# Kernel tuning notes

Measured on AMD Instinct MI355X. Metric: run time of the kernel, lower is better.

Reference implementation:

```python
import jax, jax.numpy as jnp
import numpy as np
from jax import lax

HEADS = 8
WIN = 4
SR = 4

def setup_inputs() -> dict:
    key = jax.random.key(0)
    ks = jax.random.split(key, 12)
    B, C, H, W = 8, 256, 64, 64
    def n(k, shape, s=0.02):
        return jax.random.normal(k, shape, jnp.float32) * s
    return {
        'x_bchw': jax.random.normal(ks[0], (B, C, H, W), jnp.float32),
        'W_lepe': n(ks[1], (C, C)), 'b_lepe': jnp.zeros((C,), jnp.float32),
        'conv_w': n(ks[2], (C, 1, 3, 3), 0.1), 'conv_b': jnp.zeros((C,), jnp.float32),
        'sr_w': n(ks[3], (C, C, SR, SR), 0.05), 'sr_b': jnp.zeros((C,), jnp.float32),
        'norm_g': jnp.ones((C,), jnp.float32), 'norm_b': jnp.zeros((C,), jnp.float32),
        'Wq1': n(ks[4], (C, C // 2)), 'Wkv1': n(ks[5], (C, C)),
        'Wq2': n(ks[6], (C, C // 2)), 'Wkv2': n(ks[7], (C, C)),
        'Wproj': n(ks[8], (C, C)), 'bproj': jnp.zeros((C,), jnp.float32),
        'sigma': jnp.array([2e-4], jnp.float32), 'magnitude': jnp.array([1e-2], jnp.float32),
    }

def _forward(x, W_lepe, b_lepe, conv_w, conv_b, sr_w, sr_b, norm_g, norm_b,
             Wq1, Wkv1, Wq2, Wkv2, Wproj, bproj, sigma, magnitude):
    B, C, H, W = x.shape
    N = H * W
    h2 = HEADS // 2
    d = C // HEADS
    scale = d ** -0.5
    dn = ('NCHW', 'OIHW', 'NCHW')

    tokens = x.reshape(B, C, N).transpose(0, 2, 1)  # [B,N,C]

    # LEPE: linear -> depthwise 3x3 conv
    lepe = tokens @ W_lepe + b_lepe
    lepe = lepe.transpose(0, 2, 1).reshape(B, C, H, W)
    lepe = lax.conv_general_dilated(lepe, conv_w, (1, 1), 'SAME',
                                    dimension_numbers=dn, feature_group_count=C)
    lepe = lepe + conv_b[None, :, None, None]
    lepe = lepe.reshape(B, C, N).transpose(0, 2, 1)  # [B,N,C]

    # --- global branch: spatially reduced KV ---
    q_g = (tokens @ Wq1).reshape(B, N, h2, d).transpose(0, 2, 1, 3)  # [B,h2,N,d]
    fr = lax.conv_general_dilated(x, sr_w, (SR, SR), 'VALID', dimension_numbers=dn)
    fr = fr + sr_b[None, :, None, None]
    Nr = (H // SR) * (W // SR)
    fr = fr.reshape(B, C, Nr).transpose(0, 2, 1)  # [B,Nr,C]
    mu = fr.mean(-1, keepdims=True)
    var = jnp.mean((fr - mu) ** 2, -1, keepdims=True)
    fr = (fr - mu) / jnp.sqrt(var + 1e-5) * norm_g + norm_b
    fr = jax.nn.gelu(fr, approximate=False)
    kv = (fr @ Wkv1).reshape(B, Nr, 2, h2, d)
    kg = kv[:, :, 0].transpose(0, 2, 1, 3)  # [B,h2,Nr,d]
    vg = kv[:, :, 1].transpose(0, 2, 1, 3)
    ag = jax.nn.softmax(jnp.einsum('bhnd,bhmd->bhnm', q_g, kg) * scale, axis=-1)
    xg = jnp.einsum('bhnm,bhmd->bhnd', ag, vg).transpose(0, 2, 1, 3).reshape(B, N, C // 2)
    gsig = lax.stop_gradient(ag).mean(1).mean(2).reshape(B, H, W)

    # --- local branch: 4x4 window attention ---
    qn = (tokens @ Wq2).reshape(B, N, h2, d).transpose(0, 2, 1, 3)
    kv2 = (tokens @ Wkv2).reshape(B, N, 2, h2, d)
    kl = kv2[:, :, 0].transpose(0, 2, 1, 3)
    vl = kv2[:, :, 1].transpose(0, 2, 1, 3)

    def wpart(t):
        return t.reshape(B * h2, H // WIN, WIN, W // WIN, WIN, d) \
                .transpose(0, 1, 3, 2, 4, 5).reshape(-1, WIN * WIN, d)

    al = jax.nn.softmax(jnp.einsum('wid,wjd->wij', wpart(qn), wpart(kl)) * scale, axis=-1)
    xl = jnp.einsum('wij,wjd->wid', al, wpart(vl))
    nW = (H // WIN) * (W // WIN)
    # window_reverse
    xl = xl.reshape(B, h2, H // WIN, W // WIN, WIN, WIN, d) \
           .transpose(0, 2, 4, 3, 5, 1, 6).reshape(B, N, h2 * d)
    lsig = lax.stop_gradient(al).reshape(B, h2, nW, WIN * WIN, WIN * WIN).mean(1).mean(2)
    lsig = lsig.reshape(B, H // WIN, W // WIN, WIN, WIN) \
               .transpose(0, 1, 3, 2, 4).reshape(B, H, W)

    fused = (jnp.concatenate([xg, xl], axis=-1) + lepe) @ Wproj + bproj  # [B,N,C]

    se = (lsig + gsig) * 0.5
    if H // SR == 16:  # static python condition -> apply Gaussian frequency bias (side=64)
        coord = jnp.arange(64, dtype=jnp.float32) - 31.5
        Xg, Yg = jnp.meshgrid(coord, coord, indexing='ij')
        Z = magnitude[0] * sigma[0] / (2.0 * np.pi) * jnp.exp(-0.5 * sigma[0] * (Xg * Xg + Yg * Yg)) + 1.0
        se = se * Z[None]
    se1 = se.reshape(B, N)
    se2 = se.transpose(0, 2, 1).reshape(B, N)
    return fused, se1, se2

def reference(x_bchw, W_lepe, b_lepe, conv_w, conv_b, sr_w, sr_b, norm_g, norm_b,
              Wq1, Wkv1, Wq2, Wkv2, Wproj, bproj, sigma, magnitude):
    return _forward(x_bchw, W_lepe, b_lepe, conv_w, conv_b, sr_w, sr_b, norm_g, norm_b,
                    Wq1, Wkv1, Wq2, Wkv2, Wproj, bproj, sigma, magnitude)
```

## Files before the change

kernel.cpp:

```cpp
#include <hip/hip_runtime.h>
#include <hip/hip_bf16.h>
#include <math.h>


#define SCALE 0.17677669529663687f
#define WFENCE() asm volatile("s_waitcnt lgkmcnt(0)" ::: "memory")

typedef unsigned short ush;
typedef __attribute__((ext_vector_type(8))) short s8v;
typedef __attribute__((ext_vector_type(4))) float f4v;

__device__ __forceinline__ float bf2f(ush u) {
    return __uint_as_float(((unsigned)u) << 16);
}
__device__ __forceinline__ ush f2bf(float f) {
    unsigned u = __float_as_uint(f);
    u += 0x7FFFu + ((u >> 16) & 1u);
    return (ush)(u >> 16);
}

__device__ __forceinline__ float ldfr(const void* b, size_t i, bool isbf) {
    return isbf ? bf2f(((const ush*)b)[i]) : ((const float*)b)[i];
}
__device__ __forceinline__ void ld8r(const void* b, size_t i, float* o, bool isbf) {
    if (isbf) {
        uint4 u = *reinterpret_cast<const uint4*>((const ush*)b + i);
        o[0] = bf2f((ush)u.x); o[1] = bf2f((ush)(u.x >> 16));
        o[2] = bf2f((ush)u.y); o[3] = bf2f((ush)(u.y >> 16));
        o[4] = bf2f((ush)u.z); o[5] = bf2f((ush)(u.z >> 16));
        o[6] = bf2f((ush)u.w); o[7] = bf2f((ush)(u.w >> 16));
    } else {
        const float4* p = reinterpret_cast<const float4*>((const float*)b + i);
        float4 a = p[0], c = p[1];
        o[0] = a.x; o[1] = a.y; o[2] = a.z; o[3] = a.w;
        o[4] = c.x; o[5] = c.y; o[6] = c.z; o[7] = c.w;
    }
}

struct US8 { ush s[8]; };
__device__ __forceinline__ US8 load8i(const ush* p) {
    uint4 u = *reinterpret_cast<const uint4*>(p);
    US8 r;
    r.s[0] = (ush)u.x; r.s[1] = (ush)(u.x >> 16);
    r.s[2] = (ush)u.y; r.s[3] = (ush)(u.y >> 16);
    r.s[4] = (ush)u.z; r.s[5] = (ush)(u.z >> 16);
    r.s[6] = (ush)u.w; r.s[7] = (ush)(u.w >> 16);
    return r;
}

__global__ __launch_bounds__(256) void prep(
        const void* x, const void* Wlepe, const void* Wq1, const void* Wq2,
        const void* Wkv2, const void* Wproj, const void* Wkv1, const void* blepe,
        const void* bproj, const void* convw, const void* convb, const void* srw,
        const void* srb, const void* ng, const void* nb,
        ush* tok, ush* wallt, ush* wprojt, ush* wkv1c, ush* wsrt, ush* bias_all,
        ush* bprojc, ush* convwc, ush* convbc, float* srbc, float* ngc, float* nbc) {
    bool isbf = (*(const unsigned*)ng) == 0x3F803F80u;
    __shared__ float T[32][33];
    int blk = blockIdx.x, t = threadIdx.x;
    if (blk < 768) {
        int n = blk;
        const void* s; int ncols, col;
        if (n < 256)      { s = Wlepe; ncols = 256; col = n; }
        else if (n < 384) { s = Wq1;   ncols = 128; col = n - 256; }
        else if (n < 512) { s = Wq2;   ncols = 128; col = n - 384; }
        else              { s = Wkv2;  ncols = 256; col = n - 512; }
        wallt[n * 256 + t] = f2bf(ldfr(s, (size_t)t * ncols + col, isbf));
    } else if (blk < 1024) {
        int n = blk - 768;
        wprojt[n * 256 + t] = f2bf(ldfr(Wproj, (size_t)t * 256 + n, isbf));
    } else if (blk == 1024) {
        bias_all[t]       = f2bf(ldfr(blepe, t, isbf));
        bias_all[256 + t] = 0;
        bias_all[512 + t] = 0;
        bprojc[t] = f2bf(ldfr(bproj, t, isbf));
        convbc[t] = f2bf(ldfr(convb, t, isbf));
        srbc[t] = ldfr(srb, t, isbf);
        ngc[t]  = ldfr(ng, t, isbf);
        nbc[t]  = ldfr(nb, t, isbf);
#pragma unroll
        for (int j = 0; j < 9; j++) convwc[j * 256 + t] = f2bf(ldfr(convw, t * 9 + j, isbf));
    } else if (blk < 1089) {
        int base = (blk - 1025) * 1024;
#pragma unroll
        for (int j = 0; j < 4; j++) {
            int e = base + j * 256 + t;
            wkv1c[e] = f2bf(ldfr(Wkv1, e, isbf));
        }
    } else if (blk < 1345) {
        int n = blk - 1089;
        float v[16];
        ld8r(srw, (size_t)n * 4096 + t * 16, v, isbf);
        ld8r(srw, (size_t)n * 4096 + t * 16 + 8, v + 8, isbf);
#pragma unroll
        for (int kyx = 0; kyx < 16; kyx++)
            wsrt[(size_t)n * 4096 + kyx * 256 + t] = f2bf(v[kyx]);
    } else {
        int blk2 = blk - 1345;
        int n0 = (blk2 & 127) * 32, c0 = ((blk2 >> 7) & 7) * 32, b = blk2 >> 10;
        int cl = t >> 5, nl = t & 31;
#pragma unroll
        for (int i = 0; i < 4; i++) {
            int c = c0 + cl + i * 8;
            T[cl + i * 8][nl] = ldfr(x, (((size_t)(b * 256 + c)) << 12) + n0 + nl, isbf);
        }
        __syncthreads();
        int cl2 = t & 31, nr = t >> 5;
#pragma unroll
        for (int i = 0; i < 4; i++) {
            int n = n0 + nr + i * 8;
            tok[(size_t)(b * 4096 + n) * 256 + c0 + cl2] = f2bf(T[cl2][nr + i * 8]);
        }
    }
}

__global__ __launch_bounds__(256) void big_gemm(const ush* __restrict__ tok,
                                                const ush* __restrict__ wsrt,
                                                const ush* __restrict__ wallt,
                                                const ush* __restrict__ bias_all,
                                                float* __restrict__ fr_part,
                                                ush* __restrict__ lepe_lin,
                                                ush* __restrict__ qg,
                                                ush* __restrict__ qn,
                                                ush* __restrict__ kv2) {
    __shared__ ush As[128][40];
    __shared__ ush Bs[128][40];
    int t = threadIdx.x, blk = blockIdx.x;
    int r = t >> 1, half = t & 1;
    int lane = t & 63, wv = t >> 6;
    int moff = (wv & 1) * 64, noff = (wv >> 1) * 64;
    int fm = lane & 15, q8 = (lane >> 4) * 8;
    int row4 = (lane >> 4) * 4;
    f4v acc[4][4] = {};
    if (blk < 128) {
        int m0 = (blk & 15) * 128, jt = (blk >> 4) & 1, kz = blk >> 5;
        int m = m0 + r;
        int b = m >> 8, p = m & 255;
        size_t abase = ((size_t)(b * 4096 + (p >> 4) * 256 + (p & 15) * 4)) * 256 + half * 16;
        const ush* bsrc = wsrt + (size_t)(jt * 128 + r) * 4096 + half * 16;
        for (int j = 0; j < 32; j++) {
            int k0 = kz * 1024 + j * 32;
            int kyx = k0 >> 8, ci0 = k0 & 255;
            int ky = kyx >> 2, kx = kyx & 3;
            const ush* asrc = tok + abase + (size_t)(ky * 64 + kx) * 256 + ci0;
            uint4 a0 = *reinterpret_cast<const uint4*>(asrc);
            uint4 a1 = *reinterpret_cast<const uint4*>(asrc + 8);
            uint4 b0 = *reinterpret_cast<const uint4*>(bsrc + k0);
            uint4 b1 = *reinterpret_cast<const uint4*>(bsrc + k0 + 8);
            *reinterpret_cast<uint4*>(&As[r][half * 16])     = a0;
            *reinterpret_cast<uint4*>(&As[r][half * 16 + 8]) = a1;
            *reinterpret_cast<uint4*>(&Bs[r][half * 16])     = b0;
            *reinterpret_cast<uint4*>(&Bs[r][half * 16 + 8]) = b1;
            __syncthreads();
            s8v af[4], bfr[4];
#pragma unroll
            for (int mi = 0; mi < 4; mi++)
                af[mi] = *reinterpret_cast<const s8v*>(&As[moff + mi * 16 + fm][q8]);
#pragma unroll
            for (int ni = 0; ni < 4; ni++)
                bfr[ni] = *reinterpret_cast<const s8v*>(&Bs[noff + ni * 16 + fm][q8]);
#pragma unroll
            for (int mi = 0; mi < 4; mi++)
#pragma unroll
                for (int ni = 0; ni < 4; ni++)
                    acc[mi][ni] = __builtin_amdgcn_mfma_f32_16x16x32_bf16(af[mi], bfr[ni], acc[mi][ni], 0, 0, 0);
            __syncthreads();
        }
#pragma unroll
        for (int mi = 0; mi < 4; mi++)
#pragma unroll
            for (int ni = 0; ni < 4; ni++) {
                int ncol = jt * 128 + noff + ni * 16 + fm;
                f4v c = acc[mi][ni];
#pragma unroll
                for (int rr = 0; rr < 4; rr++) {
                    int mm = m0 + moff + mi * 16 + row4 + rr;
                    fr_part[((size_t)kz * 2048 + mm) * 256 + ncol] = c[rr];
                }
            }
    } else {
        int blk2 = blk - 128;
        int m0 = (blk2 & 255) * 128, jt = blk2 >> 8;
        const ush* asrc = tok + (size_t)(m0 + r) * 256 + half * 16;
        const ush* bsrc = wallt + (size_t)(jt * 128 + r) * 256 + half * 16;
        for (int k0 = 0; k0 < 256; k0 += 32) {
            uint4 a0 = *reinterpret_cast<const uint4*>(asrc + k0);
            uint4 a1 = *reinterpret_cast<const uint4*>(asrc + k0 + 8);
            uint4 b0 = *reinterpret_cast<const uint4*>(bsrc + k0);
            uint4 b1 = *reinterpret_cast<const uint4*>(bsrc + k0 + 8);
            *reinterpret_cast<uint4*>(&As[r][half * 16])     = a0;
            *reinterpret_cast<uint4*>(&As[r][half * 16 + 8]) = a1;
            *reinterpret_cast<uint4*>(&Bs[r][half * 16])     = b0;
            *reinterpret_cast<uint4*>(&Bs[r][half * 16 + 8]) = b1;
            __syncthreads();
            s8v af[4], bfr[4];
#pragma unroll
            for (int mi = 0; mi < 4; mi++)
                af[mi] = *reinterpret_cast<const s8v*>(&As[moff + mi * 16 + fm][q8]);
#pragma unroll
            for (int ni = 0; ni < 4; ni++)
                bfr[ni] = *reinterpret_cast<const s8v*>(&Bs[noff + ni * 16 + fm][q8]);
#pragma unroll
            for (int mi = 0; mi < 4; mi++)
#pragma unroll
                for (int ni = 0; ni < 4; ni++)
                    acc[mi][ni] = __builtin_amdgcn_mfma_f32_16x16x32_bf16(af[mi], bfr[ni], acc[mi][ni], 0, 0, 0);
            __syncthreads();
        }
        ush* dst; int stride, colbase;
        if (jt == 0)      { dst = lepe_lin; stride = 256; colbase = 0; }
        else if (jt == 1) { dst = lepe_lin; stride = 256; colbase = 128; }
        else if (jt == 2) { dst = qg;       stride = 128; colbase = 0; }
        else if (jt == 3) { dst = qn;       stride = 128; colbase = 0; }
        else if (jt == 4) { dst = kv2;      stride = 256; colbase = 0; }
        else              { dst = kv2;      stride = 256; colbase = 128; }
#pragma unroll
        for (int mi = 0; mi < 4; mi++)
#pragma unroll
            for (int ni = 0; ni < 4; ni++) {
                int ncol = noff + ni * 16 + fm;
                float bias = bf2f(bias_all[jt * 128 + ncol]);
                f4v c = acc[mi][ni];
#pragma unroll
                for (int rr = 0; rr < 4; rr++) {
                    int m = m0 + moff + mi * 16 + row4 + rr;
                    dst[(size_t)m * stride + colbase + ncol] = f2bf(c[rr] + bias);
                }
            }
    }
}

__global__ __launch_bounds__(256) void ln_gelu_red(const float* __restrict__ fr_part,
                                                   const float* __restrict__ srbc,
                                                   const float* __restrict__ ngc,
                                                   const float* __restrict__ nbc,
                                                   float* __restrict__ fr) {
    __shared__ float rs[256], rq[256];
    int row = blockIdx.x, t = threadIdx.x;
    float v = srbc[t];
#pragma unroll
    for (int kz = 0; kz < 4; kz++)
        v += fr_part[((size_t)kz * 2048 + row) * 256 + t];
    rs[t] = v; rq[t] = v * v;
    __syncthreads();
    for (int s = 128; s > 0; s >>= 1) {
        if (t < s) { rs[t] += rs[t + s]; rq[t] += rq[t + s]; }
        __syncthreads();
    }
    float mu = rs[0] * (1.f / 256.f);
    float var = rq[0] * (1.f / 256.f) - mu * mu;
    float xn = (v - mu) * rsqrtf(var + 1e-5f);
    float y = xn * ngc[t] + nbc[t];
    float ge = 0.5f * y * (1.f + erff(y * 0.70710678118654752f));
    fr[(size_t)row * 256 + t] = ge;
}

__device__ __forceinline__ void mm_inner(const float (*As)[68], const float (*Bs)[68],
                                         float (*acc)[4], int tx, int ty) {
#pragma unroll
    for (int k = 0; k < 32; k++) {
        float a[4], bv[4];
#pragma unroll
        for (int ii = 0; ii < 4; ii++) a[ii] = As[k][ty * 4 + ii];
#pragma unroll
        for (int jj = 0; jj < 4; jj++) bv[jj] = Bs[k][tx * 4 + jj];
#pragma unroll
        for (int ii = 0; ii < 4; ii++)
#pragma unroll
            for (int jj = 0; jj < 4; jj++)
                acc[ii][jj] = fmaf(a[ii], bv[jj], acc[ii][jj]);
    }
}

__global__ __launch_bounds__(256) void gemm_fr(const float* __restrict__ A,
                                               const ush* __restrict__ Wm,
                                               ush* __restrict__ Kbf,
                                               ush* __restrict__ Vtb) {
    __shared__ float As[32][68];
    __shared__ float Bs[32][68];
    int t = threadIdx.x;
    int m0 = blockIdx.x * 64, j0 = blockIdx.y * 64;
    int i = t & 63, kq0 = (t >> 6) * 8;
    int kkB = t >> 3, jB0 = (t & 7) * 8;
    int tx = t & 15, ty = t >> 4;
    float acc[4][4] = {};
    for (int k0 = 0; k0 < 256; k0 += 32) {
        const float* ap = A + (size_t)(m0 + i) * 256 + k0 + kq0;
#pragma unroll
        for (int q = 0; q < 8; q++) As[kq0 + q][i] = ap[q];
        US8 bv = load8i(Wm + (size_t)(k0 + kkB) * 256 + j0 + jB0);
#pragma unroll
        for (int q = 0; q < 8; q++) Bs[kkB][jB0 + q] = bf2f(bv.s[q]);
        __syncthreads();
        mm_inner(As, Bs, acc, tx, ty);
        __syncthreads();
    }
#pragma unroll
    for (int ii = 0; ii < 4; ii++) {
        int m = m0 + ty * 4 + ii;
        int b = m >> 8, kv = m & 255;
#pragma unroll
        for (int jj = 0; jj < 4; jj++) {
            int j = j0 + tx * 4 + jj;
            ush v = f2bf(acc[ii][jj]);
            if (j < 128) {
                int h = j >> 5, d = j & 31;
                Kbf[(((size_t)(b * 4 + h) * 256) + kv) * 32 + d] = v;
            } else {
                int j2 = j - 128;
                int h = j2 >> 5, d = j2 & 31;
                Vtb[(((size_t)(b * 4 + h) * 32) + d) * 256 + kv] = v;
            }
        }
    }
}

__global__ __launch_bounds__(256) void gatt(const ush* __restrict__ qg,
                                            const ush* __restrict__ Kbf,
                                            const ush* __restrict__ Vtb,
                                            ush* __restrict__ xg) {
    __shared__ ush Ks[256][40];
    __shared__ ush Vt[32][264];
    __shared__ ush Ps[4][64][40];
    __shared__ float ls[4][64];
    int t = threadIdx.x;
    int bh = blockIdx.x & 31, yt = blockIdx.x >> 5;
    int wv = t >> 6, lane = t & 63, quad = lane >> 4, fm = lane & 15, q8 = quad * 8;
    {
        const uint4* ksrc = reinterpret_cast<const uint4*>(Kbf + ((size_t)bh * 256 + t) * 32);
#pragma unroll
        for (int i = 0; i < 4; i++)
            *reinterpret_cast<uint4*>(&Ks[t][i * 8]) = ksrc[i];
        const uint4* vsrc = reinterpret_cast<const uint4*>(Vtb + ((size_t)bh * 32 + (t >> 3)) * 256 + (t & 7) * 32);
#pragma unroll
        for (int i = 0; i < 4; i++)
            *reinterpret_cast<uint4*>(&Vt[t >> 3][(t & 7) * 32 + i * 8]) = vsrc[i];
    }
    __syncthreads();
    int b = bh >> 2, h = bh & 3;
    int q0 = yt * 256 + wv * 64;
    s8v qb[4];
#pragma unroll
    for (int nt = 0; nt < 4; nt++)
        qb[nt] = *reinterpret_cast<const s8v*>(
            qg + ((size_t)(b * 4096 + q0 + nt * 16 + fm)) * 128 + h * 32 + q8);
    f4v accO[4][2] = {};
    float lsum[4] = {};
    for (int c = 0; c < 8; c++) {
        int kv0 = c * 32;
        f4v sa[2][4];
#pragma unroll
        for (int mt = 0; mt < 2; mt++) {
            s8v kf = *reinterpret_cast<const s8v*>(&Ks[kv0 + mt * 16 + fm][q8]);
#pragma unroll
            for (int nt = 0; nt < 4; nt++)
                sa[mt][nt] = __builtin_amdgcn_mfma_f32_16x16x32_bf16(
                    kf, qb[nt], (f4v){0.f, 0.f, 0.f, 0.f}, 0, 0, 0);
        }
        if (c) WFENCE();
#pragma unroll
        for (int nt = 0; nt < 4; nt++) {
#pragma unroll
            for (int mt = 0; mt < 2; mt++) {
                f4v v = sa[mt][nt];
                float e0 = __expf(v[0] * SCALE);
                float e1 = __expf(v[1] * SCALE);
                float e2 = __expf(v[2] * SCALE);
                float e3 = __expf(v[3] * SCALE);
                lsum[nt] += (e0 + e1) + (e2 + e3);
                unsigned p0 = (unsigned)f2bf(e0) | ((unsigned)f2bf(e1) << 16);
                unsigned p1 = (unsigned)f2bf(e2) | ((unsigned)f2bf(e3) << 16);
                *reinterpret_cast<uint2*>(&Ps[wv][nt * 16 + fm][mt * 16 + quad * 4]) =
                    make_uint2(p0, p1);
            }
        }
        WFENCE();
#pragma unroll
        for (int qt = 0; qt < 4; qt++) {
            s8v pf = *reinterpret_cast<const s8v*>(&Ps[wv][qt * 16 + fm][q8]);
#pragma unroll
            for (int dt = 0; dt < 2; dt++) {
                s8v vf = *reinterpret_cast<const s8v*>(&Vt[dt * 16 + fm][kv0 + q8]);
                accO[qt][dt] = __builtin_amdgcn_mfma_f32_16x16x32_bf16(pf, vf, accO[qt][dt], 0, 0, 0);
            }
        }
    }
#pragma unroll
    for (int nt = 0; nt < 4; nt++) {
        float r = lsum[nt];
        r += __shfl_xor(r, 16, 64);
        r += __shfl_xor(r, 32, 64);
        if (quad == 0) ls[wv][nt * 16 + fm] = r;
    }
    WFENCE();
#pragma unroll
    for (int qt = 0; qt < 4; qt++) {
#pragma unroll
        for (int r = 0; r < 4; r++) {
            int qrow = qt * 16 + quad * 4 + r;
            float inv = 1.f / ls[wv][qrow];
            size_t base = ((size_t)(b * 4096 + q0 + qrow)) * 128 + h * 32;
            xg[base + fm]      = f2bf(accO[qt][0][r] * inv);
            xg[base + 16 + fm] = f2bf(accO[qt][1][r] * inv);
        }
    }
}

__global__ __launch_bounds__(256) void latt_dw(const ush* __restrict__ qn,
                                               const ush* __restrict__ kv2,
                                               const ush* __restrict__ lepe_lin,
                                               const ush* __restrict__ cw,
                                               const ush* __restrict__ cb,
                                               ush* __restrict__ xl,
                                               float* __restrict__ lsig,
                                               ush* __restrict__ lepe) {
    int blk = blockIdx.x, t = threadIdx.x;
    if (blk < 512) {
        int i = t & 15, h = (t >> 4) & 3, sub = t >> 6;
        int widx = blk * 4 + sub;
        int bidx = widx >> 8, w = widx & 255;
        int wy = w >> 4, wx = w & 15;
        int nbase = (wy * 4) * 64 + wx * 4;
        int ni = nbase + (i >> 2) * 64 + (i & 3);
        float q[32];
        {
            const ush* qp = qn + (size_t)(bidx * 4096 + ni) * 128 + h * 32;
#pragma unroll
            for (int dd = 0; dd < 32; dd += 8) {
                US8 v = load8i(qp + dd);
#pragma unroll
                for (int q2 = 0; q2 < 8; q2++) q[dd + q2] = bf2f(v.s[q2]);
            }
        }
        float s[16];
#pragma unroll
        for (int j = 0; j < 16; j++) {
            int nj = nbase + (j >> 2) * 64 + (j & 3);
            const ush* kp = kv2 + (size_t)(bidx * 4096 + nj) * 256 + h * 32;
            float acc = 0.f;
#pragma unroll
            for (int dd = 0; dd < 32; dd += 8) {
                US8 v = load8i(kp + dd);
#pragma unroll
                for (int q2 = 0; q2 < 8; q2++) acc = fmaf(q[dd + q2], bf2f(v.s[q2]), acc);
            }
            s[j] = acc * SCALE;
        }
        float mx = s[0];
#pragma unroll
        for (int j = 1; j < 16; j++) mx = fmaxf(mx, s[j]);
        float l = 0.f;
#pragma unroll
        for (int j = 0; j < 16; j++) { s[j] = __expf(s[j] - mx); l += s[j]; }
        float inv = 1.f / l;
#pragma unroll
        for (int j = 0; j < 16; j++) s[j] *= inv;
#pragma unroll
        for (int j = 0; j < 16; j++) {
            float r = s[j];
#pragma unroll
            for (int off = 1; off < 64; off <<= 1) r += __shfl_xor(r, off, 64);
            if ((t & 63) == 0) lsig[(size_t)(bidx * 256 + w) * 16 + j] = r * (1.f / 64.f);
        }
        float acc[32] = {};
#pragma unroll
        for (int j = 0; j < 16; j++) {
            int nj = nbase + (j >> 2) * 64 + (j & 3);
            const ush* vp = kv2 + (size_t)(bidx * 4096 + nj) * 256 + 128 + h * 32;
#pragma unroll
            for (int dd = 0; dd < 32; dd += 8) {
                US8 v = load8i(vp + dd);
#pragma unroll
                for (int q2 = 0; q2 < 8; q2++) acc[dd + q2] = fmaf(s[j], bf2f(v.s[q2]), acc[dd + q2]);
            }
        }
        ush* op = xl + (size_t)(bidx * 4096 + ni) * 128 + h * 32;
#pragma unroll
        for (int dd = 0; dd < 32; dd++) op[dd] = f2bf(acc[dd]);
    } else {
        int idx = (blk - 512) * 256 + t;
        int c0 = (idx & 31) * 8;
        int m = idx >> 5;
        int n = m & 4095;
        int h = n >> 6, w = n & 63;
        int mb = m - n;
        float acc[8];
        {
            US8 bv = load8i(cb + c0);
#pragma unroll
            for (int q = 0; q < 8; q++) acc[q] = bf2f(bv.s[q]);
        }
#pragma unroll
        for (int dy = -1; dy <= 1; dy++) {
            int hh = h + dy;
            if (hh < 0 || hh > 63) continue;
#pragma unroll
            for (int dx = -1; dx <= 1; dx++) {
                int ww = w + dx;
                if (ww < 0 || ww > 63) continue;
                US8 wv8 = load8i(cw + ((dy + 1) * 3 + (dx + 1)) * 256 + c0);
                US8 xv = load8i(lepe_lin + (size_t)(mb + hh * 64 + ww) * 256 + c0);
#pragma unroll
                for (int q = 0; q < 8; q++)
                    acc[q] = fmaf(bf2f(xv.s[q]), bf2f(wv8.s[q]), acc[q]);
            }
        }
        unsigned pk[4];
#pragma unroll
        for (int q = 0; q < 4; q++)
            pk[q] = (unsigned)f2bf(acc[2 * q]) | ((unsigned)f2bf(acc[2 * q + 1]) << 16);
        *reinterpret_cast<uint4*>(lepe + (size_t)m * 256 + c0) = make_uint4(pk[0], pk[1], pk[2], pk[3]);
    }
}

__global__ __launch_bounds__(256) void final_k(const void* __restrict__ ng,
                                               const ush* __restrict__ xg,
                                               const ush* __restrict__ xl,
                                               const ush* __restrict__ lepe,
                                               const ush* __restrict__ wprojt,
                                               const ush* __restrict__ bprojc,
                                               const float* __restrict__ lsig,
                                               const void* __restrict__ sg,
                                               const void* __restrict__ mg,
                                               void* __restrict__ out) {
    bool isbf = (*(const unsigned*)ng) == 0x3F803F80u;
    __shared__ ush As[128][40];
    __shared__ ush Bs[128][40];
    int blk = blockIdx.x, t = threadIdx.x;
    if (blk < 512) {
        int m0 = (blk & 255) * 128, jt = blk >> 8;
        int r = t >> 1, half = t & 1;
        int lane = t & 63, wv = t >> 6;
        int moff = (wv & 1) * 64, noff = (wv >> 1) * 64;
        int fm = lane & 15, q8 = (lane >> 4) * 8;
        f4v acc[4][4] = {};
        const ush* bsrc = wprojt + (size_t)(jt * 128 + r) * 256 + half * 16;
        for (int k0 = 0; k0 < 256; k0 += 32) {
            int kk = k0 + half * 16;
            const ush* s1 = (kk < 128) ? (xg + (size_t)(m0 + r) * 128 + kk)
                                       : (xl + (size_t)(m0 + r) * 128 + kk - 128);
            const ush* lp = lepe + (size_t)(m0 + r) * 256 + kk;
            US8 u0 = load8i(s1), u1 = load8i(s1 + 8);
            US8 l0 = load8i(lp), l1 = load8i(lp + 8);
            unsigned pk[8];
#pragma unroll
            for (int q = 0; q < 4; q++) {
                ush e0 = f2bf(bf2f(u0.s[2 * q]) + bf2f(l0.s[2 * q]));
                ush e1 = f2bf(bf2f(u0.s[2 * q + 1]) + bf2f(l0.s[2 * q + 1]));
                pk[q] = (unsigned)e0 | ((unsigned)e1 << 16);
                ush e2 = f2bf(bf2f(u1.s[2 * q]) + bf2f(l1.s[2 * q]));
                ush e3 = f2bf(bf2f(u1.s[2 * q + 1]) + bf2f(l1.s[2 * q + 1]));
                pk[4 + q] = (unsigned)e2 | ((unsigned)e3 << 16);
            }
            uint4 b0 = *reinterpret_cast<const uint4*>(bsrc + k0);
            uint4 b1 = *reinterpret_cast<const uint4*>(bsrc + k0 + 8);
            *reinterpret_cast<uint4*>(&As[r][half * 16])     = make_uint4(pk[0], pk[1], pk[2], pk[3]);
            *reinterpret_cast<uint4*>(&As[r][half * 16 + 8]) = make_uint4(pk[4], pk[5], pk[6], pk[7]);
            *reinterpret_cast<uint4*>(&Bs[r][half * 16])     = b0;
            *reinterpret_cast<uint4*>(&Bs[r][half * 16 + 8]) = b1;
            __syncthreads();
            s8v af[4], bfr[4];
#pragma unroll
            for (int mi = 0; mi < 4; mi++)
                af[mi] = *reinterpret_cast<const s8v*>(&As[moff + mi * 16 + fm][q8]);
#pragma unroll
            for (int ni = 0; ni < 4; ni++)
                bfr[ni] = *reinterpret_cast<const s8v*>(&Bs[noff + ni * 16 + fm][q8]);
#pragma unroll
            for (int mi = 0; mi < 4; mi++)
#pragma unroll
                for (int ni = 0; ni < 4; ni++)
                    acc[mi][ni] = __builtin_amdgcn_mfma_f32_16x16x32_bf16(af[mi], bfr[ni], acc[mi][ni], 0, 0, 0);
            __syncthreads();
        }
        int row4 = (lane >> 4) * 4;
#pragma unroll
        for (int mi = 0; mi < 4; mi++)
#pragma unroll
            for (int ni = 0; ni < 4; ni++) {
                int ncol = jt * 128 + noff + ni * 16 + fm;
                float bias = bf2f(bprojc[ncol]);
                f4v c = acc[mi][ni];
#pragma unroll
                for (int rr = 0; rr < 4; rr++) {
                    int m = m0 + moff + mi * 16 + row4 + rr;
                    float v = c[rr] + bias;
                    if (isbf) ((ush*)out)[(size_t)m * 256 + ncol] = f2bf(v);
                    else      ((float*)out)[(size_t)m * 256 + ncol] = v;
                }
            }
    } else {
        int idx = (blk - 512) * 256 + t;
        int bidx = idx >> 12, n = idx & 4095;
        int h = n >> 6, w = n & 63;
        float lsv = lsig[(size_t)(bidx * 256 + (h >> 2) * 16 + (w >> 2)) * 16 + (h & 3) * 4 + (w & 3)];
        float se = (lsv + 0.00390625f) * 0.5f;
        float sig = ldfr(sg, 0, isbf), mag = ldfr(mg, 0, isbf);
        float X = (float)h - 31.5f, Y = (float)w - 31.5f;
        float Z = mag * sig * 0.15915494309189535f * __expf(-0.5f * sig * (X * X + Y * Y)) + 1.f;
        se *= Z;
        size_t o1 = 8388608 + (size_t)bidx * 4096 + n;
        size_t o2 = 8421376 + (size_t)bidx * 4096 + w * 64 + h;
        if (isbf) { ((ush*)out)[o1] = f2bf(se); ((ush*)out)[o2] = f2bf(se); }
        else      { ((float*)out)[o1] = se;     ((float*)out)[o2] = se; }
    }
}

extern "C" void kernel_launch(void* const* d_in, const int* in_sizes, int n_in,
                              void* d_out, int out_size, void* d_ws, size_t ws_size,
                              hipStream_t stream) {
    const void* x     = d_in[0];
    const void* Wlepe = d_in[1];
    const void* blepe = d_in[2];
    const void* convw = d_in[3];
    const void* convb = d_in[4];
    const void* srw   = d_in[5];
    const void* srb   = d_in[6];
    const void* ng    = d_in[7];
    const void* nb    = d_in[8];
    const void* Wq1   = d_in[9];
    const void* Wkv1  = d_in[10];
    const void* Wq2   = d_in[11];
    const void* Wkv2  = d_in[12];
    const void* Wproj = d_in[13];
    const void* bproj = d_in[14];
    const void* sg    = d_in[15];
    const void* mg    = d_in[16];
    (void)in_sizes; (void)n_in; (void)out_size; (void)ws_size;

    char* ws = (char*)d_ws;
    ush*   tok      = (ush*)(ws + 0);
    ush*   xg       = (ush*)(ws + 0);
    ush*   xl       = (ush*)(ws + 8388608);
    ush*   lepe_lin = (ush*)(ws + 16777216);
    ush*   qg       = (ush*)(ws + 33554432);
    ush*   qn       = (ush*)(ws + 41943040);
    ush*   kv2      = (ush*)(ws + 50331648);
    float* fr       = (float*)(ws + 67108864);
    ush*   Kbf      = (ush*)(ws + 69206016);
    ush*   Vtb      = (ush*)(ws + 69730304);
    float* lsig     = (float*)(ws + 71303168);
    ush*   wallt    = (ush*)(ws + 71434256);
    ush*   wkv1c    = (ush*)(ws + 71827472);
    ush*   wprojt   = (ush*)(ws + 71958544);
    ush*   bias_all = (ush*)(ws + 72089616);
    ush*   bprojc   = (ush*)(ws + 72091152);
    ush*   convwc   = (ush*)(ws + 72091664);
    ush*   convbc   = (ush*)(ws + 72096272);
    float* srbc     = (float*)(ws + 72096784);
    float* ngc      = (float*)(ws + 72097808);
    float* nbc      = (float*)(ws + 72098832);
    ush*   lepe     = (ush*)(ws + 73400320);
    float* fr_part  = (float*)(ws + 90177536);
    ush*   wsrt     = (ush*)(ws + 98566144);

    dim3 blk(256);
    prep<<<dim3(9537), blk, 0, stream>>>(x, Wlepe, Wq1, Wq2, Wkv2, Wproj, Wkv1,
        blepe, bproj, convw, convb, srw, srb, ng, nb,
        tok, wallt, wprojt, wkv1c, wsrt, bias_all, bprojc, convwc, convbc, srbc, ngc, nbc);

    big_gemm<<<dim3(1664), blk, 0, stream>>>(tok, wsrt, wallt, bias_all,
        fr_part, lepe_lin, qg, qn, kv2);

    ln_gelu_red<<<dim3(2048), blk, 0, stream>>>(fr_part, srbc, ngc, nbc, fr);
    gemm_fr<<<dim3(32, 4), blk, 0, stream>>>(fr, wkv1c, Kbf, Vtb);

    gatt<<<dim3(512), blk, 0, stream>>>(qg, Kbf, Vtb, xg);
    latt_dw<<<dim3(4608), blk, 0, stream>>>(qn, kv2, lepe_lin, convwc, convbc,
        xl, lsig, lepe);

    final_k<<<dim3(640), blk, 0, stream>>>(ng, xg, xl, lepe, wprojt, bprojc,
        lsig, sg, mg, d_out);
}
```

Measured before the change: 286.9 us.

## Use MFMA for local window attention with transposed V from GEMM epilogue

Rewrites the local 4x4-window attention to compute QK^T and PV with bf16 16x16x32 MFMA instructions, one wave per head and one block per window, replacing scalar FMA loops. To feed the PV MFMA, the big GEMM epilogue additionally writes a transposed copy of V (per batch/head/dim, token-contiguous) into a new workspace buffer. This cuts scalar ALU work and per-thread register pressure in the local attention, but adds strided scattered 2-byte stores to the GEMM epilogue and more launched blocks. The softmax skips max subtraction and the probabilities are rounded to bf16, which slightly changes numerics.

```diff
diff --git a/kernel.cpp b/kernel.cpp
--- a/kernel.cpp
+++ b/kernel.cpp
@@ -122,7 +122,8 @@
                                                 ush* __restrict__ lepe_lin,
                                                 ush* __restrict__ qg,
                                                 ush* __restrict__ qn,
-                                                ush* __restrict__ kv2) {
+                                                ush* __restrict__ kv2,
+                                                ush* __restrict__ v2t) {
     __shared__ ush As[128][40];
     __shared__ ush Bs[128][40];
     int t = threadIdx.x, blk = blockIdx.x;
@@ -224,7 +225,13 @@
 #pragma unroll
                 for (int rr = 0; rr < 4; rr++) {
                     int m = m0 + moff + mi * 16 + row4 + rr;
-                    dst[(size_t)m * stride + colbase + ncol] = f2bf(c[rr] + bias);
+                    ush vv = f2bf(c[rr] + bias);
+                    dst[(size_t)m * stride + colbase + ncol] = vv;
+                    if (jt == 5) {
+                        int bb = m >> 12, n = m & 4095;
+                        int hh = ncol >> 5, dd = ncol & 31;
+                        v2t[(((size_t)((bb * 4 + hh) * 32 + dd)) << 12) + n] = vv;
+                    }
                 }
             }
     }
@@ -408,77 +415,78 @@
 
 __global__ __launch_bounds__(256) void latt_dw(const ush* __restrict__ qn,
                                                const ush* __restrict__ kv2,
+                                               const ush* __restrict__ v2t,
                                                const ush* __restrict__ lepe_lin,
                                                const ush* __restrict__ cw,
                                                const ush* __restrict__ cb,
                                                ush* __restrict__ xl,
                                                float* __restrict__ lsig,
                                                ush* __restrict__ lepe) {
+    __shared__ ush Ps[4][16][24];
+    __shared__ float lw[4][16];
     int blk = blockIdx.x, t = threadIdx.x;
-    if (blk < 512) {
-        int i = t & 15, h = (t >> 4) & 3, sub = t >> 6;
-        int widx = blk * 4 + sub;
-        int bidx = widx >> 8, w = widx & 255;
+    if (blk < 2048) {
+        int wv = t >> 6, lane = t & 63, quad = lane >> 4, fm = lane & 15;
+        int b = blk >> 8, w = blk & 255;
         int wy = w >> 4, wx = w & 15;
-        int nbase = (wy * 4) * 64 + wx * 4;
-        int ni = nbase + (i >> 2) * 64 + (i & 3);
-        float q[32];
-        {
-            const ush* qp = qn + (size_t)(bidx * 4096 + ni) * 128 + h * 32;
-#pragma unroll
-            for (int dd = 0; dd < 32; dd += 8) {
-                US8 v = load8i(qp + dd);
-#pragma unroll
-                for (int q2 = 0; q2 < 8; q2++) q[dd + q2] = bf2f(v.s[q2]);
-            }
-        }
-        float s[16];
-#pragma unroll
-        for (int j = 0; j < 16; j++) {
-            int nj = nbase + (j >> 2) * 64 + (j & 3);
-            const ush* kp = kv2 + (size_t)(bidx * 4096 + nj) * 256 + h * 32;
-            float acc = 0.f;
-#pragma unroll
-            for (int dd = 0; dd < 32; dd += 8) {
-                US8 v = load8i(kp + dd);
-#pragma unroll
-                for (int q2 = 0; q2 < 8; q2++) acc = fmaf(q[dd + q2], bf2f(v.s[q2]), acc);
-            }
-            s[j] = acc * SCALE;
-        }
-        float mx = s[0];
-#pragma unroll
-        for (int j = 1; j < 16; j++) mx = fmaxf(mx, s[j]);
-        float l = 0.f;
-#pragma unroll
-        for (int j = 0; j < 16; j++) { s[j] = __expf(s[j] - mx); l += s[j]; }
-        float inv = 1.f / l;
-#pragma unroll
-        for (int j = 0; j < 16; j++) s[j] *= inv;
-#pragma unroll
-        for (int j = 0; j < 16; j++) {
-            float r = s[j];
-#pragma unroll
-            for (int off = 1; off < 64; off <<= 1) r += __shfl_xor(r, off, 64);
-            if ((t & 63) == 0) lsig[(size_t)(bidx * 256 + w) * 16 + j] = r * (1.f / 64.f);
-        }
-        float acc[32] = {};
-#pragma unroll
-        for (int j = 0; j < 16; j++) {
-            int nj = nbase + (j >> 2) * 64 + (j & 3);
-            const ush* vp = kv2 + (size_t)(bidx * 4096 + nj) * 256 + 128 + h * 32;
-#pragma unroll
-            for (int dd = 0; dd < 32; dd += 8) {
-                US8 v = load8i(vp + dd);
-#pragma unroll
-                for (int q2 = 0; q2 < 8; q2++) acc[dd + q2] = fmaf(s[j], bf2f(v.s[q2]), acc[dd + q2]);
-            }
-        }
-        ush* op = xl + (size_t)(bidx * 4096 + ni) * 128 + h * 32;
-#pragma unroll
-        for (int dd = 0; dd < 32; dd++) op[dd] = f2bf(acc[dd]);
+        int nbase = wy * 256 + wx * 4;
+        int h = wv;
+        int nf = nbase + (fm >> 2) * 64 + (fm & 3);
+        s8v aq = *reinterpret_cast<const s8v*>(
+            qn + ((size_t)(b * 4096 + nf)) * 128 + h * 32 + quad * 8);
+        s8v bk = *reinterpret_cast<const s8v*>(
+            kv2 + ((size_t)(b * 4096 + nf)) * 256 + h * 32 + quad * 8);
+        f4v sa = __builtin_amdgcn_mfma_f32_16x16x32_bf16(aq, bk, (f4v){0.f, 0.f, 0.f, 0.f}, 0, 0, 0);
+        float p[4];
+        float cs = 0.f;
+#pragma unroll
+        for (int r = 0; r < 4; r++) {
+            float e = __expf(sa[r] * SCALE);
+            float s = e;
+            s += __shfl_xor(s, 1, 64);
+            s += __shfl_xor(s, 2, 64);
+            s += __shfl_xor(s, 4, 64);
+            s += __shfl_xor(s, 8, 64);
+            p[r] = e / s;
+            cs += p[r];
+            Ps[wv][quad * 4 + r][fm] = f2bf(p[r]);
+        }
+        cs += __shfl_xor(cs, 16, 64);
+        cs += __shfl_xor(cs, 32, 64);
+        if (lane < 16) lw[wv][fm] = cs;
+        WFENCE();
+        s8v zero8 = {0, 0, 0, 0, 0, 0, 0, 0};
+        s8v ap = zero8;
+        if (quad < 2)
+            ap = *reinterpret_cast<const s8v*>(&Ps[wv][fm][quad * 8]);
+        f4v o[2];
+#pragma unroll
+        for (int dt = 0; dt < 2; dt++) {
+            s8v bv = zero8;
+            if (quad < 2) {
+                const ush* vp = v2t + (((size_t)((b * 4 + h) * 32 + dt * 16 + fm)) << 12)
+                                + nbase + quad * 128;
+                uint2 lo = *reinterpret_cast<const uint2*>(vp);
+                uint2 hi = *reinterpret_cast<const uint2*>(vp + 64);
+                union { s8v v; uint2 u[2]; } pk;
+                pk.u[0] = lo; pk.u[1] = hi;
+                bv = pk.v;
+            }
+            o[dt] = __builtin_amdgcn_mfma_f32_16x16x32_bf16(ap, bv, (f4v){0.f, 0.f, 0.f, 0.f}, 0, 0, 0);
+        }
+#pragma unroll
+        for (int r = 0; r < 4; r++) {
+            int nq = nbase + quad * 64 + r;
+            ush* op = xl + ((size_t)(b * 4096 + nq)) * 128 + h * 32 + fm;
+            op[0]  = f2bf(o[0][r]);
+            op[16] = f2bf(o[1][r]);
+        }
+        __syncthreads();
+        if (t < 16)
+            lsig[((size_t)(b * 256 + w)) * 16 + t] =
+                (lw[0][t] + lw[1][t] + lw[2][t] + lw[3][t]) * (1.f / 64.f);
     } else {
-        int idx = (blk - 512) * 256 + t;
+        int idx = (blk - 2048) * 256 + t;
         int c0 = (idx & 31) * 8;
         int m = idx >> 5;
         int n = m & 4095;
@@ -653,6 +661,7 @@
     ush*   lepe     = (ush*)(ws + 73400320);
     float* fr_part  = (float*)(ws + 90177536);
     ush*   wsrt     = (ush*)(ws + 98566144);
+    ush*   v2t      = (ush*)(ws + 100663296);
 
     dim3 blk(256);
     prep<<<dim3(9537), blk, 0, stream>>>(x, Wlepe, Wq1, Wq2, Wkv2, Wproj, Wkv1,
@@ -660,13 +669,13 @@
         tok, wallt, wprojt, wkv1c, wsrt, bias_all, bprojc, convwc, convbc, srbc, ngc, nbc);
 
     big_gemm<<<dim3(1664), blk, 0, stream>>>(tok, wsrt, wallt, bias_all,
-        fr_part, lepe_lin, qg, qn, kv2);
+        fr_part, lepe_lin, qg, qn, kv2, v2t);
 
     ln_gelu_red<<<dim3(2048), blk, 0, stream>>>(fr_part, srbc, ngc, nbc, fr);
     gemm_fr<<<dim3(32, 4), blk, 0, stream>>>(fr, wkv1c, Kbf, Vtb);
 
     gatt<<<dim3(512), blk, 0, stream>>>(qg, Kbf, Vtb, xg);
-    latt_dw<<<dim3(4608), blk, 0, stream>>>(qn, kv2, lepe_lin, convwc, convbc,
+    latt_dw<<<dim3(6144), blk, 0, stream>>>(qn, kv2, v2t, lepe_lin, convwc, convbc,
         xl, lsig, lepe);
 
     final_k<<<dim3(640), blk, 0, stream>>>(ng, xg, xl, lepe, wprojt, bprojc,
```

Measured after the change: 254.6 us. 1.13x faster.
